# Optimization experiments

Hardware: AMD Instinct MI355X
Metric: run time of the kernel (lower is better)

## Reference

```python
import jax, jax.numpy as jnp
import numpy as np

N, E, CIN, H = 100000, 1600000, 128, 128


def setup_inputs() -> dict:
    key = jax.random.key(0)
    ks = jax.random.split(key, 10)
    return {
        "x": jax.random.normal(ks[0], (N, CIN), dtype=jnp.float32),
        "edge_index": jax.random.randint(ks[1], (2, E), 0, N, dtype=jnp.int64),
        "edge_weight": jax.random.uniform(ks[2], (E,), dtype=jnp.float32),
        "h_prev": jax.random.normal(ks[3], (N, H), dtype=jnp.float32),
        "c_prev": jax.random.normal(ks[4], (N, H), dtype=jnp.float32),
        "Wx0": jax.random.normal(ks[5], (4, CIN, H), dtype=jnp.float32) * 0.05,
        "Wx1": jax.random.normal(ks[6], (4, CIN, H), dtype=jnp.float32) * 0.05,
        "Wh0": jax.random.normal(ks[7], (4, H, H), dtype=jnp.float32) * 0.05,
        "Wh1": jax.random.normal(ks[8], (4, H, H), dtype=jnp.float32) * 0.05,
        "bx": jnp.zeros((4, H), dtype=jnp.float32),
        "bh": jnp.zeros((4, H), dtype=jnp.float32),
    }


def _scaled_laplacian_norm(edge_index, edge_weight, n):
    # PyG ChebConv norm with lambda_max=2.0, sym normalization:
    # L_hat = 2L/lambda_max - I = -D^{-1/2} A D^{-1/2} (zero diagonal).
    src, dst = edge_index[0], edge_index[1]
    deg = jax.ops.segment_sum(edge_weight, src, num_segments=n)
    safe = jnp.where(deg > 0, deg, 1.0)
    dis = jnp.where(deg > 0, 1.0 / jnp.sqrt(safe), 0.0)  # deg_inv_sqrt, inf->0
    norm = -(dis[src] * edge_weight * dis[dst])
    return src, dst, norm


def _propagate(feat, src, dst, norm, n):
    # (L_hat @ feat)[i] = sum_{e: dst_e=i} norm_e * feat[src_e]
    return jax.ops.segment_sum(feat[src] * norm[:, None], dst, num_segments=n)


def reference(x, edge_index, edge_weight, h_prev, c_prev, Wx0, Wx1, Wh0, Wh1, bx, bh):
    n = x.shape[0]
    src, dst, norm = _scaled_laplacian_norm(edge_index, edge_weight, n)
    # Shared Chebyshev propagation across all 4 gates (K=2: T0=I, T1=L_hat)
    Lx = _propagate(x, src, dst, norm, n)          # [N, CIN]
    Lh = _propagate(h_prev, src, dst, norm, n)     # [N, H]
    gates = (
        jnp.einsum("nc,gch->gnh", x, Wx0)
        + jnp.einsum("nc,gch->gnh", Lx, Wx1)
        + jnp.einsum("nd,gdh->gnh", h_prev, Wh0)
        + jnp.einsum("nd,gdh->gnh", Lh, Wh1)
        + bx[:, None, :] + bh[:, None, :]
    )  # [4, N, H]
    i = jax.nn.sigmoid(gates[0])
    f = jax.nn.sigmoid(gates[1])
    g = jnp.tanh(gates[2])
    o = jax.nn.sigmoid(gates[3])
    c_t = f * c_prev + i * g
    h_t = o * jnp.tanh(c_t)
    return (h_t, c_t)
```

## Files before the change

kernel.cpp:

```cpp
#include <hip/hip_runtime.h>
#include <hip/hip_bf16.h>

#define NN   100000
#define NE   1600000
#define MPAD 100096
#define BK   64

typedef __attribute__((ext_vector_type(8))) short bf16x8;
typedef __attribute__((ext_vector_type(4))) float f32x4;
typedef __attribute__((ext_vector_type(8))) unsigned short u16x8;

#define OFF_DEG    0ull
#define OFF_CUR    400384ull
#define OFF_XH     800768ull
#define OFF_FP     52049920ull
#define OFF_WT     103299072ull
#define OFF_BIAS   103823360ull

__device__ __forceinline__ unsigned short f2bf(float f) {
    unsigned int u = __float_as_uint(f);
    u += 0x7fffu + ((u >> 16) & 1u);
    return (unsigned short)(u >> 16);
}
__device__ __forceinline__ float bf2f(unsigned short u) {
    return __uint_as_float(((unsigned int)u) << 16);
}
__device__ __forceinline__ float sigf(float x)  { return 1.f / (1.f + __expf(-x)); }
__device__ __forceinline__ float tanhf_(float x){ return 1.f - 2.f / (__expf(2.f * x) + 1.f); }

typedef __attribute__((address_space(3))) void lds_void;
typedef __attribute__((address_space(1))) void g_void;
__device__ __forceinline__ void gload16(const void* g, void* l) {
    __builtin_amdgcn_global_load_lds((const g_void*)g, (lds_void*)l, 16, 0, 0);
}

__global__ void zero_kernel(float4* __restrict__ p, int n4) {
    int t = blockIdx.x * 256 + threadIdx.x;
    if (t < n4) p[t] = make_float4(0.f, 0.f, 0.f, 0.f);
}

#define EDGE_BLOCKS 6250
#define CVT_BLOCKS  25024
__global__ void mega1_kernel(const int* __restrict__ src, const int* __restrict__ dst,
                             const float* __restrict__ ew,
                             float* __restrict__ deg, int* __restrict__ cursor,
                             uint2* __restrict__ bkt,
                             const float* __restrict__ x, const float* __restrict__ hp,
                             unsigned short* __restrict__ XH,
                             const float* __restrict__ Wx0, const float* __restrict__ Wx1,
                             const float* __restrict__ Wh0, const float* __restrict__ Wh1,
                             const float* __restrict__ bx,  const float* __restrict__ bh,
                             unsigned short* __restrict__ Wt, float* __restrict__ bias) {
    int b = blockIdx.x;
    if (b < EDGE_BLOCKS) {
        int e = b * 256 + threadIdx.x;
        int s = src[e], d = dst[e];
        float w = ew[e];
        atomicAdd(&deg[s], w);
        int pos = atomicAdd(&cursor[d], 1);
        if (pos < BK) {
            uint2 v; v.x = (unsigned)s; v.y = __float_as_uint(w);
            bkt[((size_t)d << 6) + pos] = v;
        }
    } else if (b < EDGE_BLOCKS + CVT_BLOCKS) {
        int t = (b - EDGE_BLOCKS) * 256 + threadIdx.x;
        int n = t >> 6, q = t & 63;
        ushort4 o = make_ushort4(0, 0, 0, 0);
        if (n < NN) {
            const float* s = (q < 32) ? (x + (size_t)n * 128 + (q << 2))
                                      : (hp + (size_t)n * 128 + ((q - 32) << 2));
            float4 v = *(const float4*)s;
            o = make_ushort4(f2bf(v.x), f2bf(v.y), f2bf(v.z), f2bf(v.w));
        }
        *(ushort4*)(XH + (size_t)n * 256 + (q << 2)) = o;
    } else {
        int t = (b - EDGE_BLOCKS - CVT_BLOCKS) * 256 + threadIdx.x;
        int col = t >> 9, k = t & 511;
        int h = col >> 2, g = col & 3;
        const float* W; int kk;
        if      (k < 128) { W = Wx0; kk = k; }
        else if (k < 256) { W = Wx1; kk = k - 128; }
        else if (k < 384) { W = Wh0; kk = k - 256; }
        else              { W = Wh1; kk = k - 384; }
        float v = W[((size_t)(g << 7) + kk) * 128 + h];
        Wt[(size_t)col * 512 + k] = f2bf(v);
        if (k == 0) bias[col] = bx[(g << 7) + h] + bh[(g << 7) + h];
    }
}

__launch_bounds__(256)
__global__ void gather_pack_kernel(const float* __restrict__ deg,
                                   const int* __restrict__ cursor,
                                   const uint2* __restrict__ bkt,
                                   const unsigned short* __restrict__ XH,
                                   unsigned short* __restrict__ Fp) {
    int node = (blockIdx.x * 256 + threadIdx.x) >> 6;
    int lane = threadIdx.x & 63;
    if (node >= MPAD) return;
    const int g  = lane >> 4;
    const int li = lane & 15;
    unsigned short* Frow = Fp + (size_t)node * 256;
    if (node >= NN) {
        if (g < 2) *(uint4*)(Frow + li * 16 + g * 8) = make_uint4(0, 0, 0, 0);
        return;
    }
    int cnt = cursor[node];
    cnt = cnt > BK ? BK : cnt;
    float dd = deg[node];
    float disd = dd > 0.f ? rsqrtf(dd) : 0.f;
    const uint2* row = bkt + ((size_t)node << 6);
    float acc[16];
#pragma unroll
    for (int k = 0; k < 16; ++k) acc[k] = 0.f;

    int e = g;
    uint2 ce;
    if (e < cnt) ce = row[e];
    while (e < cnt) {
        uint2 cur = ce;
        int en = e + 4;
        if (en < cnt) ce = row[en];
        float dsv = deg[cur.x];
        const unsigned short* xr = XH + (size_t)cur.x * 256 + li * 16;
        u16x8 v0 = *(const u16x8*)(xr);
        u16x8 v1 = *(const u16x8*)(xr + 8);
        float diss = dsv > 0.f ? rsqrtf(dsv) : 0.f;
        float nm = -(diss * __uint_as_float(cur.y) * disd);
#pragma unroll
        for (int k = 0; k < 8; ++k) acc[k]     += nm * bf2f((unsigned short)v0[k]);
#pragma unroll
        for (int k = 0; k < 8; ++k) acc[k + 8] += nm * bf2f((unsigned short)v1[k]);
        e = en;
    }
#pragma unroll
    for (int k = 0; k < 16; ++k) {
        acc[k] += __shfl_xor(acc[k], 16, 64);
        acc[k] += __shfl_xor(acc[k], 32, 64);
    }
    if (g < 2) {
        u16x8 o;
#pragma unroll
        for (int k = 0; k < 8; ++k)
            o[k] = f2bf((g & 1) ? acc[k + 8] : acc[k]);
        *(u16x8*)(Frow + li * 16 + g * 8) = o;
    }
}

__device__ __forceinline__ f32x4 shflx4(f32x4 v, int m) {
    f32x4 r;
    r[0] = __shfl_xor(v[0], m, 64);
    r[1] = __shfl_xor(v[1], m, 64);
    r[2] = __shfl_xor(v[2], m, 64);
    r[3] = __shfl_xor(v[3], m, 64);
    return r;
}
__device__ __forceinline__ float sel4(f32x4 v, int k) {
    float r = v[0];
    r = (k == 1) ? v[1] : r;
    r = (k == 2) ? v[2] : r;
    r = (k == 3) ? v[3] : r;
    return r;
}
__device__ __forceinline__ float pick4(float a0, float a1, float a2, float a3, int k) {
    float r = a0;
    r = (k == 1) ? a1 : r;
    r = (k == 2) ? a2 : r;
    r = (k == 3) ? a3 : r;
    return r;
}

#define WAITV(n)  asm volatile("s_waitcnt vmcnt(" #n ")" ::: "memory")
#define WAITLGKM0 asm volatile("s_waitcnt lgkmcnt(0)" ::: "memory")

__launch_bounds__(256)
__global__ void gemm_lstm_kernel(const unsigned short* __restrict__ XHu,
                                 const unsigned short* __restrict__ Fpu,
                                 const unsigned short* __restrict__ Wtu,
                                 const float* __restrict__ bias,
                                 const float* __restrict__ c_prev,
                                 float* __restrict__ out) {
    __shared__ __align__(16) short sa[4 * 4096];
    __shared__ __align__(16) short sb[4 * 4096];

    const int tid  = threadIdx.x;
    const int lane = tid & 63;
    const int wave = tid >> 6;
    const int wm = wave >> 1, wn = wave & 1;
    const int lr = lane & 15, lq = lane >> 4;

    const int b = blockIdx.x;
    const int ntile = (b >> 3) & 3;
    const int mtile = (b & 7) | ((b >> 5) << 3);
    if (mtile >= 782) return;
    const size_t m0 = (size_t)mtile * 128;
    const int n0 = ntile * 128;

    const short* XH = (const short*)XHu;
    const short* Fp = (const short*)Fpu;
    const short* Wt = (const short*)Wtu;

    const int arow = tid >> 2;
    const int sx   = (((tid & 3) ^ ((arow >> 1) & 3)) << 3);
    const size_t rowA = (m0 + arow) * 256 + sx;
    const short* gB = Wt + (size_t)(n0 + arow) * 512 + sx;

    const int rbase = wm * 64 + lq * 4 + (lr & 3);
    const int hbase = (n0 >> 2) + wn * 16 + (lr >> 2);

    const int xr = (lr >> 1) & 3;
    int offA[4], offB[4];
#pragma unroll
    for (int i = 0; i < 4; ++i) {
        offA[i] = (wm * 64 + i * 16 + lr) * 32 + ((lq ^ xr) << 3);
        offB[i] = (wn * 64 + i * 16 + lr) * 32 + ((lq ^ xr) << 3);
    }

    f32x4 acc[4][4];
#pragma unroll
    for (int i = 0; i < 4; ++i)
#pragma unroll
        for (int j = 0; j < 4; ++j) acc[i][j] = (f32x4){0.f, 0.f, 0.f, 0.f};

    auto stage = [&](int kt) {
        const int buf = (kt & 3) << 12;
        const int off = ((kt >> 3) << 7) + ((kt & 3) << 5);
        const short* Ab = ((kt >> 2) & 1) ? Fp : XH;
        gload16(Ab + rowA + off,            &sa[buf + wave * 512]);
        gload16(Ab + rowA + 64 * 256 + off, &sa[buf + 2048 + wave * 512]);
        gload16(gB + kt * 32,               &sb[buf + wave * 512]);
        gload16(gB + kt * 32 + 64 * 512,    &sb[buf + 2048 + wave * 512]);
    };

    stage(0); stage(1); stage(2);

#pragma unroll
    for (int kt = 0; kt < 16; ++kt) {
        if      (kt <= 13) WAITV(8);
        else if (kt == 14) WAITV(4);
        else               WAITV(0);
        __builtin_amdgcn_sched_barrier(0);
        __builtin_amdgcn_s_barrier();
        if (kt + 3 < 16) stage(kt + 3);
        const int buf = (kt & 3) << 12;
        bf16x8 af[4], bfr[4];
#pragma unroll
        for (int i = 0; i < 4; ++i) af[i]  = *(const bf16x8*)&sa[buf + offA[i]];
#pragma unroll
        for (int i = 0; i < 4; ++i) bfr[i] = *(const bf16x8*)&sb[buf + offB[i]];
        __builtin_amdgcn_s_setprio(1);
#pragma unroll
        for (int i = 0; i < 4; ++i)
#pragma unroll
            for (int j = 0; j < 4; ++j)
                acc[i][j] = __builtin_amdgcn_mfma_f32_16x16x32_bf16(af[i], bfr[j], acc[i][j], 0, 0, 0);
        __builtin_amdgcn_s_setprio(0);
        WAITLGKM0;
        __builtin_amdgcn_sched_barrier(0);
    }

    float bs[4];
#pragma unroll
    for (int j = 0; j < 4; ++j) bs[j] = bias[n0 + wn * 64 + j * 16 + lr];
    float cp[4][4];
#pragma unroll
    for (int i = 0; i < 4; ++i) {
        size_t grow = m0 + rbase + i * 16;
#pragma unroll
        for (int j = 0; j < 4; ++j)
            cp[i][j] = (grow < NN) ? c_prev[grow * 128 + hbase + j * 4] : 0.f;
    }

    const int k = lr & 3;
#pragma unroll
    for (int i = 0; i < 4; ++i) {
        size_t grow = m0 + rbase + i * 16;
        if (grow >= NN) continue;
#pragma unroll
        for (int j = 0; j < 4; ++j) {
            f32x4 v0 = acc[i][j];
            v0[0] += bs[j]; v0[1] += bs[j]; v0[2] += bs[j]; v0[3] += bs[j];
            f32x4 v1 = shflx4(v0, 1);
            f32x4 v2 = shflx4(v0, 2);
            f32x4 v3 = shflx4(v0, 3);
            float vv0 = sel4(v0, k), vv1 = sel4(v1, k),
                  vv2 = sel4(v2, k), vv3 = sel4(v3, k);
            float gi = pick4(vv0, vv1, vv2, vv3, k);
            float gf = pick4(vv0, vv1, vv2, vv3, k ^ 1);
            float gg = pick4(vv0, vv1, vv2, vv3, k ^ 2);
            float go = pick4(vv0, vv1, vv2, vv3, k ^ 3);
            float iv = sigf(gi), fv = sigf(gf), gv = tanhf_(gg), ov = sigf(go);
            float ct = fv * cp[i][j] + iv * gv;
            float ht = ov * tanhf_(ct);
            int h = hbase + j * 4;
            out[grow * 128 + h] = ht;
            out[(size_t)NN * 128 + grow * 128 + h] = ct;
        }
    }
}

extern "C" void kernel_launch(void* const* d_in, const int* in_sizes, int n_in,
                              void* d_out, int out_size, void* d_ws, size_t ws_size,
                              hipStream_t stream) {
    const float* x      = (const float*)d_in[0];
    const int*   ei     = (const int*)  d_in[1];
    const float* ew     = (const float*)d_in[2];
    const float* h_prev = (const float*)d_in[3];
    const float* c_prev = (const float*)d_in[4];
    const float* Wx0    = (const float*)d_in[5];
    const float* Wx1    = (const float*)d_in[6];
    const float* Wh0    = (const float*)d_in[7];
    const float* Wh1    = (const float*)d_in[8];
    const float* bx     = (const float*)d_in[9];
    const float* bh     = (const float*)d_in[10];
    float* out = (float*)d_out;

    char* ws = (char*)d_ws;
    float*          deg    = (float*)(ws + OFF_DEG);
    int*            cursor = (int*)  (ws + OFF_CUR);
    unsigned short* XH     = (unsigned short*)(ws + OFF_XH);
    unsigned short* Fp     = (unsigned short*)(ws + OFF_FP);
    unsigned short* Wt     = (unsigned short*)(ws + OFF_WT);
    float*          bias   = (float*)(ws + OFF_BIAS);
    uint2*          bkt    = (uint2*)d_out;

    const int* src = ei;
    const int* dst = ei + NE;

    zero_kernel<<<(50048 + 255) / 256, 256, 0, stream>>>((float4*)ws, 50048);

    mega1_kernel<<<EDGE_BLOCKS + CVT_BLOCKS + 1024, 256, 0, stream>>>(
        src, dst, ew, deg, cursor, bkt, x, h_prev, XH,
        Wx0, Wx1, Wh0, Wh1, bx, bh, Wt, bias);

    gather_pack_kernel<<<MPAD / 4, 256, 0, stream>>>(deg, cursor, bkt, XH, Fp);

    gemm_lstm_kernel<<<3136, 256, 0, stream>>>(XH, Fp, Wt, bias, c_prev, out);
}
```

Before: 600.9 us.

## Split GEMM: compute unpropagated half early, overlapped with edge bucketing

```diff
diff --git a/kernel.cpp b/kernel.cpp
--- a/kernel.cpp
+++ b/kernel.cpp
@@ -10,12 +10,14 @@
 typedef __attribute__((ext_vector_type(4))) float f32x4;
 typedef __attribute__((ext_vector_type(8))) unsigned short u16x8;
 
-#define OFF_DEG    0ull
-#define OFF_CUR    400384ull
-#define OFF_XH     800768ull
-#define OFF_FP     52049920ull
-#define OFF_WT     103299072ull
-#define OFF_BIAS   103823360ull
+#define OFF_DEG  0ull
+#define OFF_CUR  400384ull
+#define OFF_XH   800768ull
+#define OFF_FP   52049920ull
+#define OFF_WT   103299072ull
+#define OFF_BIAS 103823360ull
+#define OFF_GP   103825408ull
+#define WS_NEED  206323712ull
 
 __device__ __forceinline__ unsigned short f2bf(float f) {
     unsigned int u = __float_as_uint(f);
@@ -34,26 +36,60 @@
     __builtin_amdgcn_global_load_lds((const g_void*)g, (lds_void*)l, 16, 0, 0);
 }
 
-__global__ void zero_kernel(float4* __restrict__ p, int n4) {
-    int t = blockIdx.x * 256 + threadIdx.x;
-    if (t < n4) p[t] = make_float4(0.f, 0.f, 0.f, 0.f);
-}
-
-#define EDGE_BLOCKS 6250
-#define CVT_BLOCKS  25024
-__global__ void mega1_kernel(const int* __restrict__ src, const int* __restrict__ dst,
+__global__ void zero_packw_kernel(float4* __restrict__ z,
+                                  const float* __restrict__ Wx0, const float* __restrict__ Wx1,
+                                  const float* __restrict__ Wh0, const float* __restrict__ Wh1,
+                                  const float* __restrict__ bx,  const float* __restrict__ bh,
+                                  unsigned short* __restrict__ Wt, float* __restrict__ bias) {
+    int b = blockIdx.x;
+    if (b < 196) {
+        int t = b * 256 + threadIdx.x;
+        if (t < 50048) z[t] = make_float4(0.f, 0.f, 0.f, 0.f);
+        return;
+    }
+    int t = (b - 196) * 256 + threadIdx.x;
+    int col = t >> 9, k = t & 511;
+    int h = col >> 2, g = col & 3;
+    const float* W; int kk;
+    if      (k < 128) { W = Wx0; kk = k; }
+    else if (k < 256) { W = Wx1; kk = k - 128; }
+    else if (k < 384) { W = Wh0; kk = k - 256; }
+    else              { W = Wh1; kk = k - 384; }
+    float v = W[((size_t)(g << 7) + kk) * 128 + h];
+    Wt[(size_t)col * 512 + k] = f2bf(v);
+    if (k == 0) bias[col] = bx[(g << 7) + h] + bh[(g << 7) + h];
+}
+
+#define MIX_BLOCKS 9408
+#define CVT_BLOCKS 25024
+__global__ void mega2_kernel(const int* __restrict__ src, const int* __restrict__ dst,
                              const float* __restrict__ ew,
                              float* __restrict__ deg, int* __restrict__ cursor,
                              uint2* __restrict__ bkt,
                              const float* __restrict__ x, const float* __restrict__ hp,
                              unsigned short* __restrict__ XH,
-                             const float* __restrict__ Wx0, const float* __restrict__ Wx1,
-                             const float* __restrict__ Wh0, const float* __restrict__ Wh1,
-                             const float* __restrict__ bx,  const float* __restrict__ bh,
-                             unsigned short* __restrict__ Wt, float* __restrict__ bias) {
-    int b = blockIdx.x;
-    if (b < EDGE_BLOCKS) {
-        int e = b * 256 + threadIdx.x;
+                             const unsigned short* __restrict__ Wtu,
+                             unsigned short* __restrict__ Gp,
+                             int with_g1) {
+    __shared__ __align__(16) short s1a[2][4096];
+    __shared__ __align__(16) short s1b[2][4096];
+
+    const int b = blockIdx.x;
+    int eid = -1, g1 = -1, cvt = -1;
+    if (with_g1) {
+        if (b < MIX_BLOCKS) {
+            int r = b % 3, g = b / 3;
+            if (r == 0) g1 = g;
+            else if (g < 3125) eid = (r - 1) * 3125 + g;
+            else return;
+        } else cvt = b - MIX_BLOCKS;
+    } else {
+        if (b < 6250) eid = b;
+        else cvt = b - 6250;
+    }
+
+    if (eid >= 0) {
+        int e = eid * 256 + threadIdx.x;
         int s = src[e], d = dst[e];
         float w = ew[e];
         atomicAdd(&deg[s], w);
@@ -62,8 +98,10 @@
             uint2 v; v.x = (unsigned)s; v.y = __float_as_uint(w);
             bkt[((size_t)d << 6) + pos] = v;
         }
-    } else if (b < EDGE_BLOCKS + CVT_BLOCKS) {
-        int t = (b - EDGE_BLOCKS) * 256 + threadIdx.x;
+        return;
+    }
+    if (cvt >= 0) {
+        int t = cvt * 256 + threadIdx.x;
         int n = t >> 6, q = t & 63;
         ushort4 o = make_ushort4(0, 0, 0, 0);
         if (n < NN) {
@@ -73,19 +111,98 @@
             o = make_ushort4(f2bf(v.x), f2bf(v.y), f2bf(v.z), f2bf(v.w));
         }
         *(ushort4*)(XH + (size_t)n * 256 + (q << 2)) = o;
-    } else {
-        int t = (b - EDGE_BLOCKS - CVT_BLOCKS) * 256 + threadIdx.x;
-        int col = t >> 9, k = t & 511;
-        int h = col >> 2, g = col & 3;
-        const float* W; int kk;
-        if      (k < 128) { W = Wx0; kk = k; }
-        else if (k < 256) { W = Wx1; kk = k - 128; }
-        else if (k < 384) { W = Wh0; kk = k - 256; }
-        else              { W = Wh1; kk = k - 384; }
-        float v = W[((size_t)(g << 7) + kk) * 128 + h];
-        Wt[(size_t)col * 512 + k] = f2bf(v);
-        if (k == 0) bias[col] = bx[(g << 7) + h] + bh[(g << 7) + h];
-    }
+        return;
+    }
+
+    const int ntile = (g1 >> 3) & 3;
+    const int mtile = (g1 & 7) | ((g1 >> 5) << 3);
+    if (mtile >= 782) return;
+    const size_t m0 = (size_t)mtile * 128;
+    const int n0 = ntile * 128;
+
+    const int tid  = threadIdx.x;
+    const int lane = tid & 63;
+    const int wave = tid >> 6;
+    const int wm = wave >> 1, wn = wave & 1;
+    const int lr = lane & 15, lq = lane >> 4;
+
+    const short* Wt = (const short*)Wtu;
+    const int ar  = tid >> 2;
+    const int ac  = tid & 3;
+    const int sxw = ((ac ^ ((ar >> 1) & 3)) << 3);
+    const short* gB = Wt + (size_t)(n0 + ar) * 512 + sxw;
+
+    const int xr = (lr >> 1) & 3;
+    int offA[4], offB[4];
+#pragma unroll
+    for (int i = 0; i < 4; ++i) {
+        offA[i] = (wm * 64 + i * 16 + lr) * 32 + ((lq ^ xr) << 3);
+        offB[i] = (wn * 64 + i * 16 + lr) * 32 + ((lq ^ xr) << 3);
+    }
+
+    f32x4 acc[4][4];
+#pragma unroll
+    for (int i = 0; i < 4; ++i)
+#pragma unroll
+        for (int j = 0; j < 4; ++j) acc[i][j] = (f32x4){0.f, 0.f, 0.f, 0.f};
+
+    auto ldsA = [&](int s, int buf) {
+#pragma unroll
+        for (int half = 0; half < 2; ++half) {
+            int row = ar + half * 64;
+            size_t grow = m0 + row;
+            float v[8];
+            if (grow < NN) {
+                const float* p = (s < 4 ? x + grow * 128 + s * 32
+                                        : hp + grow * 128 + (s - 4) * 32) + ac * 8;
+                float4 a0 = *(const float4*)p;
+                float4 a1 = *(const float4*)(p + 4);
+                v[0] = a0.x; v[1] = a0.y; v[2] = a0.z; v[3] = a0.w;
+                v[4] = a1.x; v[5] = a1.y; v[6] = a1.z; v[7] = a1.w;
+            } else {
+#pragma unroll
+                for (int q = 0; q < 8; ++q) v[q] = 0.f;
+            }
+            u16x8 o;
+#pragma unroll
+            for (int q = 0; q < 8; ++q) o[q] = f2bf(v[q]);
+            *(u16x8*)&s1a[buf][row * 32 + sxw] = o;
+        }
+    };
+    auto stB = [&](int s, int buf) {
+        int ktw = (s < 4) ? s : s + 4;
+        gload16(gB + ktw * 32,            &s1b[buf][wave * 512]);
+        gload16(gB + ktw * 32 + 64 * 512, &s1b[buf][2048 + wave * 512]);
+    };
+
+    stB(0, 0); ldsA(0, 0);
+    __syncthreads();
+    for (int s = 0; s < 8; ++s) {
+        const int buf = s & 1;
+        if (s < 7) { stB(s + 1, buf ^ 1); ldsA(s + 1, buf ^ 1); }
+        bf16x8 af[4], bfr[4];
+#pragma unroll
+        for (int i = 0; i < 4; ++i) af[i]  = *(const bf16x8*)&s1a[buf][offA[i]];
+#pragma unroll
+        for (int i = 0; i < 4; ++i) bfr[i] = *(const bf16x8*)&s1b[buf][offB[i]];
+#pragma unroll
+        for (int i = 0; i < 4; ++i)
+#pragma unroll
+            for (int j = 0; j < 4; ++j)
+                acc[i][j] = __builtin_amdgcn_mfma_f32_16x16x32_bf16(af[i], bfr[j], acc[i][j], 0, 0, 0);
+        __syncthreads();
+    }
+
+#pragma unroll
+    for (int i = 0; i < 4; ++i)
+#pragma unroll
+        for (int j = 0; j < 4; ++j) {
+            int col = n0 + wn * 64 + j * 16 + lr;
+            size_t rowb = m0 + wm * 64 + i * 16 + lq * 4;
+            ushort4 o = make_ushort4(f2bf(acc[i][j][0]), f2bf(acc[i][j][1]),
+                                     f2bf(acc[i][j][2]), f2bf(acc[i][j][3]));
+            *(ushort4*)(Gp + (size_t)col * MPAD + rowb) = o;
+        }
 }
 
 __launch_bounds__(256)
@@ -172,12 +289,14 @@
 #define WAITV(n)  asm volatile("s_waitcnt vmcnt(" #n ")" ::: "memory")
 #define WAITLGKM0 asm volatile("s_waitcnt lgkmcnt(0)" ::: "memory")
 
+template <int SPLIT>
 __launch_bounds__(256)
 __global__ void gemm_lstm_kernel(const unsigned short* __restrict__ XHu,
                                  const unsigned short* __restrict__ Fpu,
                                  const unsigned short* __restrict__ Wtu,
                                  const float* __restrict__ bias,
                                  const float* __restrict__ c_prev,
+                                 const unsigned short* __restrict__ Gp,
                                  float* __restrict__ out) {
     __shared__ __align__(16) short sa[4 * 4096];
     __shared__ __align__(16) short sb[4 * 4096];
@@ -215,14 +334,8 @@
         offB[i] = (wn * 64 + i * 16 + lr) * 32 + ((lq ^ xr) << 3);
     }
 
-    f32x4 acc[4][4];
-#pragma unroll
-    for (int i = 0; i < 4; ++i)
-#pragma unroll
-        for (int j = 0; j < 4; ++j) acc[i][j] = (f32x4){0.f, 0.f, 0.f, 0.f};
-
-    auto stage = [&](int kt) {
-        const int buf = (kt & 3) << 12;
+    auto stage = [&](int kt, int b4) {
+        const int buf = b4 << 12;
         const int off = ((kt >> 3) << 7) + ((kt & 3) << 5);
         const short* Ab = ((kt >> 2) & 1) ? Fp : XH;
         gload16(Ab + rowA + off,            &sa[buf + wave * 512]);
@@ -230,18 +343,43 @@
         gload16(gB + kt * 32,               &sb[buf + wave * 512]);
         gload16(gB + kt * 32 + 64 * 512,    &sb[buf + 2048 + wave * 512]);
     };
-
-    stage(0); stage(1); stage(2);
-
-#pragma unroll
-    for (int kt = 0; kt < 16; ++kt) {
-        if      (kt <= 13) WAITV(8);
-        else if (kt == 14) WAITV(4);
-        else               WAITV(0);
+    auto ktOf = [&](int s) { return SPLIT ? (s < 4 ? s + 4 : s + 8) : s; };
+    const int NS = SPLIT ? 8 : 16;
+
+    f32x4 acc[4][4];
+    if (SPLIT) {
+        ushort4 gpt[4][4];
+#pragma unroll
+        for (int i = 0; i < 4; ++i)
+#pragma unroll
+            for (int j = 0; j < 4; ++j)
+                gpt[i][j] = *(const ushort4*)(Gp +
+                    (size_t)(n0 + wn * 64 + j * 16 + lr) * MPAD +
+                    (m0 + wm * 64 + i * 16 + lq * 4));
+        stage(ktOf(0), 0); stage(ktOf(1), 1); stage(ktOf(2), 2);
+#pragma unroll
+        for (int i = 0; i < 4; ++i)
+#pragma unroll
+            for (int j = 0; j < 4; ++j)
+                acc[i][j] = (f32x4){bf2f(gpt[i][j].x), bf2f(gpt[i][j].y),
+                                    bf2f(gpt[i][j].z), bf2f(gpt[i][j].w)};
+    } else {
+#pragma unroll
+        for (int i = 0; i < 4; ++i)
+#pragma unroll
+            for (int j = 0; j < 4; ++j) acc[i][j] = (f32x4){0.f, 0.f, 0.f, 0.f};
+        stage(0, 0); stage(1, 1); stage(2, 2);
+    }
+
+#pragma unroll
+    for (int s = 0; s < NS; ++s) {
+        if      (s <= NS - 3) WAITV(8);
+        else if (s == NS - 2) WAITV(4);
+        else                  WAITV(0);
         __builtin_amdgcn_sched_barrier(0);
         __builtin_amdgcn_s_barrier();
-        if (kt + 3 < 16) stage(kt + 3);
-        const int buf = (kt & 3) << 12;
+        if (s + 3 < NS) stage(ktOf(s + 3), (s + 3) & 3);
+        const int buf = (s & 3) << 12;
         bf16x8 af[4], bfr[4];
 #pragma unroll
         for (int i = 0; i < 4; ++i) af[i]  = *(const bf16x8*)&sa[buf + offA[i]];
@@ -321,18 +459,26 @@
     unsigned short* Fp     = (unsigned short*)(ws + OFF_FP);
     unsigned short* Wt     = (unsigned short*)(ws + OFF_WT);
     float*          bias   = (float*)(ws + OFF_BIAS);
+    unsigned short* Gp     = (unsigned short*)(ws + OFF_GP);
     uint2*          bkt    = (uint2*)d_out;
 
     const int* src = ei;
     const int* dst = ei + NE;
 
-    zero_kernel<<<(50048 + 255) / 256, 256, 0, stream>>>((float4*)ws, 50048);
-
-    mega1_kernel<<<EDGE_BLOCKS + CVT_BLOCKS + 1024, 256, 0, stream>>>(
-        src, dst, ew, deg, cursor, bkt, x, h_prev, XH,
-        Wx0, Wx1, Wh0, Wh1, bx, bh, Wt, bias);
-
-    gather_pack_kernel<<<MPAD / 4, 256, 0, stream>>>(deg, cursor, bkt, XH, Fp);
-
-    gemm_lstm_kernel<<<3136, 256, 0, stream>>>(XH, Fp, Wt, bias, c_prev, out);
-}
+    const bool big = (ws_size >= WS_NEED);
+
+    zero_packw_kernel<<<196 + 1024, 256, 0, stream>>>(
+        (float4*)ws, Wx0, Wx1, Wh0, Wh1, bx, bh, Wt, bias);
+
+    if (big) {
+        mega2_kernel<<<MIX_BLOCKS + CVT_BLOCKS, 256, 0, stream>>>(
+            src, dst, ew, deg, cursor, bkt, x, h_prev, XH, Wt, Gp, 1);
+        gather_pack_kernel<<<MPAD / 4, 256, 0, stream>>>(deg, cursor, bkt, XH, Fp);
+        gemm_lstm_kernel<1><<<3136, 256, 0, stream>>>(XH, Fp, Wt, bias, c_prev, Gp, out);
+    } else {
+        mega2_kernel<<<6250 + CVT_BLOCKS, 256, 0, stream>>>(
+            src, dst, ew, deg, cursor, bkt, x, h_prev, XH, Wt, Gp, 0);
+        gather_pack_kernel<<<MPAD / 4, 256, 0, stream>>>(deg, cursor, bkt, XH, Fp);
+        gemm_lstm_kernel<0><<<3136, 256, 0, stream>>>(XH, Fp, Wt, bias, c_prev, Gp, out);
+    }
+}
```

Result: slower. 670.4 us (+11.6%).

## Widen gather edge parallelism, batch edge atomics, and move weight packing into zero kernel

Applied to the files above, without the earlier changes.

```diff
diff --git a/kernel.cpp b/kernel.cpp
--- a/kernel.cpp
+++ b/kernel.cpp
@@ -10,12 +10,12 @@
 typedef __attribute__((ext_vector_type(4))) float f32x4;
 typedef __attribute__((ext_vector_type(8))) unsigned short u16x8;
 
-#define OFF_DEG    0ull
-#define OFF_CUR    400384ull
-#define OFF_XH     800768ull
-#define OFF_FP     52049920ull
-#define OFF_WT     103299072ull
-#define OFF_BIAS   103823360ull
+#define OFF_DEG  0ull
+#define OFF_CUR  400384ull
+#define OFF_XH   800768ull
+#define OFF_FP   52049920ull
+#define OFF_WT   103299072ull
+#define OFF_BIAS 103823360ull
 
 __device__ __forceinline__ unsigned short f2bf(float f) {
     unsigned int u = __float_as_uint(f);
@@ -34,58 +34,73 @@
     __builtin_amdgcn_global_load_lds((const g_void*)g, (lds_void*)l, 16, 0, 0);
 }
 
-__global__ void zero_kernel(float4* __restrict__ p, int n4) {
-    int t = blockIdx.x * 256 + threadIdx.x;
-    if (t < n4) p[t] = make_float4(0.f, 0.f, 0.f, 0.f);
-}
-
-#define EDGE_BLOCKS 6250
-#define CVT_BLOCKS  25024
+__global__ void zero_packw_kernel(float4* __restrict__ z,
+                                  const float* __restrict__ Wx0, const float* __restrict__ Wx1,
+                                  const float* __restrict__ Wh0, const float* __restrict__ Wh1,
+                                  const float* __restrict__ bx,  const float* __restrict__ bh,
+                                  unsigned short* __restrict__ Wt, float* __restrict__ bias) {
+    int b = blockIdx.x;
+    if (b < 196) {
+        int t = b * 256 + threadIdx.x;
+        if (t < 50048) z[t] = make_float4(0.f, 0.f, 0.f, 0.f);
+        return;
+    }
+    int t = (b - 196) * 256 + threadIdx.x;
+    int col = t >> 9, k = t & 511;
+    int h = col >> 2, g = col & 3;
+    const float* W; int kk;
+    if      (k < 128) { W = Wx0; kk = k; }
+    else if (k < 256) { W = Wx1; kk = k - 128; }
+    else if (k < 384) { W = Wh0; kk = k - 256; }
+    else              { W = Wh1; kk = k - 384; }
+    float v = W[((size_t)(g << 7) + kk) * 128 + h];
+    Wt[(size_t)col * 512 + k] = f2bf(v);
+    if (k == 0) bias[col] = bx[(g << 7) + h] + bh[(g << 7) + h];
+}
+
+#define EB 1563
+#define CVT_BLOCKS 25024
 __global__ void mega1_kernel(const int* __restrict__ src, const int* __restrict__ dst,
                              const float* __restrict__ ew,
                              float* __restrict__ deg, int* __restrict__ cursor,
                              uint2* __restrict__ bkt,
                              const float* __restrict__ x, const float* __restrict__ hp,
-                             unsigned short* __restrict__ XH,
-                             const float* __restrict__ Wx0, const float* __restrict__ Wx1,
-                             const float* __restrict__ Wh0, const float* __restrict__ Wh1,
-                             const float* __restrict__ bx,  const float* __restrict__ bh,
-                             unsigned short* __restrict__ Wt, float* __restrict__ bias) {
+                             unsigned short* __restrict__ XH) {
     int b = blockIdx.x;
-    if (b < EDGE_BLOCKS) {
-        int e = b * 256 + threadIdx.x;
-        int s = src[e], d = dst[e];
-        float w = ew[e];
-        atomicAdd(&deg[s], w);
-        int pos = atomicAdd(&cursor[d], 1);
-        if (pos < BK) {
-            uint2 v; v.x = (unsigned)s; v.y = __float_as_uint(w);
-            bkt[((size_t)d << 6) + pos] = v;
+    if (b < EB) {
+        int e0 = b * 1024 + threadIdx.x;
+        int sarr[4], darr[4]; float warr[4]; bool ok[4];
+#pragma unroll
+        for (int k = 0; k < 4; ++k) {
+            int e = e0 + k * 256;
+            ok[k] = (e < NE);
+            if (ok[k]) { sarr[k] = src[e]; darr[k] = dst[e]; warr[k] = ew[e]; }
         }
-    } else if (b < EDGE_BLOCKS + CVT_BLOCKS) {
-        int t = (b - EDGE_BLOCKS) * 256 + threadIdx.x;
-        int n = t >> 6, q = t & 63;
-        ushort4 o = make_ushort4(0, 0, 0, 0);
-        if (n < NN) {
-            const float* s = (q < 32) ? (x + (size_t)n * 128 + (q << 2))
-                                      : (hp + (size_t)n * 128 + ((q - 32) << 2));
-            float4 v = *(const float4*)s;
-            o = make_ushort4(f2bf(v.x), f2bf(v.y), f2bf(v.z), f2bf(v.w));
-        }
-        *(ushort4*)(XH + (size_t)n * 256 + (q << 2)) = o;
-    } else {
-        int t = (b - EDGE_BLOCKS - CVT_BLOCKS) * 256 + threadIdx.x;
-        int col = t >> 9, k = t & 511;
-        int h = col >> 2, g = col & 3;
-        const float* W; int kk;
-        if      (k < 128) { W = Wx0; kk = k; }
-        else if (k < 256) { W = Wx1; kk = k - 128; }
-        else if (k < 384) { W = Wh0; kk = k - 256; }
-        else              { W = Wh1; kk = k - 384; }
-        float v = W[((size_t)(g << 7) + kk) * 128 + h];
-        Wt[(size_t)col * 512 + k] = f2bf(v);
-        if (k == 0) bias[col] = bx[(g << 7) + h] + bh[(g << 7) + h];
-    }
+#pragma unroll
+        for (int k = 0; k < 4; ++k)
+            if (ok[k]) atomicAdd(&deg[sarr[k]], warr[k]);
+        int pos[4];
+#pragma unroll
+        for (int k = 0; k < 4; ++k)
+            if (ok[k]) pos[k] = atomicAdd(&cursor[darr[k]], 1);
+#pragma unroll
+        for (int k = 0; k < 4; ++k)
+            if (ok[k] && pos[k] < BK) {
+                uint2 v; v.x = (unsigned)sarr[k]; v.y = __float_as_uint(warr[k]);
+                bkt[((size_t)darr[k] << 6) + pos[k]] = v;
+            }
+        return;
+    }
+    int t = (b - EB) * 256 + threadIdx.x;
+    int n = t >> 6, q = t & 63;
+    ushort4 o = make_ushort4(0, 0, 0, 0);
+    if (n < NN) {
+        const float* s = (q < 32) ? (x + (size_t)n * 128 + (q << 2))
+                                  : (hp + (size_t)n * 128 + ((q - 32) << 2));
+        float4 v = *(const float4*)s;
+        o = make_ushort4(f2bf(v.x), f2bf(v.y), f2bf(v.z), f2bf(v.w));
+    }
+    *(ushort4*)(XH + (size_t)n * 256 + (q << 2)) = o;
 }
 
 __launch_bounds__(256)
@@ -97,11 +112,11 @@
     int node = (blockIdx.x * 256 + threadIdx.x) >> 6;
     int lane = threadIdx.x & 63;
     if (node >= MPAD) return;
-    const int g  = lane >> 4;
-    const int li = lane & 15;
+    const int g  = lane >> 3;
+    const int li = lane & 7;
     unsigned short* Frow = Fp + (size_t)node * 256;
     if (node >= NN) {
-        if (g < 2) *(uint4*)(Frow + li * 16 + g * 8) = make_uint4(0, 0, 0, 0);
+        if (g < 4) *(uint4*)(Frow + li * 32 + g * 8) = make_uint4(0, 0, 0, 0);
         return;
     }
     int cnt = cursor[node];
@@ -109,40 +124,47 @@
     float dd = deg[node];
     float disd = dd > 0.f ? rsqrtf(dd) : 0.f;
     const uint2* row = bkt + ((size_t)node << 6);
-    float acc[16];
-#pragma unroll
-    for (int k = 0; k < 16; ++k) acc[k] = 0.f;
+    float acc[32];
+#pragma unroll
+    for (int k = 0; k < 32; ++k) acc[k] = 0.f;
 
     int e = g;
     uint2 ce;
     if (e < cnt) ce = row[e];
     while (e < cnt) {
         uint2 cur = ce;
-        int en = e + 4;
+        int en = e + 8;
         if (en < cnt) ce = row[en];
         float dsv = deg[cur.x];
-        const unsigned short* xr = XH + (size_t)cur.x * 256 + li * 16;
+        const unsigned short* xr = XH + (size_t)cur.x * 256 + li * 32;
         u16x8 v0 = *(const u16x8*)(xr);
         u16x8 v1 = *(const u16x8*)(xr + 8);
+        u16x8 v2 = *(const u16x8*)(xr + 16);
+        u16x8 v3 = *(const u16x8*)(xr + 24);
         float diss = dsv > 0.f ? rsqrtf(dsv) : 0.f;
         float nm = -(diss * __uint_as_float(cur.y) * disd);
 #pragma unroll
-        for (int k = 0; k < 8; ++k) acc[k]     += nm * bf2f((unsigned short)v0[k]);
-#pragma unroll
-        for (int k = 0; k < 8; ++k) acc[k + 8] += nm * bf2f((unsigned short)v1[k]);
+        for (int k = 0; k < 8; ++k) acc[k]      += nm * bf2f((unsigned short)v0[k]);
+#pragma unroll
+        for (int k = 0; k < 8; ++k) acc[k + 8]  += nm * bf2f((unsigned short)v1[k]);
+#pragma unroll
+        for (int k = 0; k < 8; ++k) acc[k + 16] += nm * bf2f((unsigned short)v2[k]);
+#pragma unroll
+        for (int k = 0; k < 8; ++k) acc[k + 24] += nm * bf2f((unsigned short)v3[k]);
         e = en;
     }
 #pragma unroll
-    for (int k = 0; k < 16; ++k) {
+    for (int k = 0; k < 32; ++k) {
+        acc[k] += __shfl_xor(acc[k], 8, 64);
         acc[k] += __shfl_xor(acc[k], 16, 64);
         acc[k] += __shfl_xor(acc[k], 32, 64);
     }
-    if (g < 2) {
+    if (g < 4) {
         u16x8 o;
 #pragma unroll
         for (int k = 0; k < 8; ++k)
-            o[k] = f2bf((g & 1) ? acc[k + 8] : acc[k]);
-        *(u16x8*)(Frow + li * 16 + g * 8) = o;
+            o[k] = f2bf(acc[g * 8 + k]);
+        *(u16x8*)(Frow + li * 32 + g * 8) = o;
     }
 }
 
@@ -326,11 +348,11 @@
     const int* src = ei;
     const int* dst = ei + NE;
 
-    zero_kernel<<<(50048 + 255) / 256, 256, 0, stream>>>((float4*)ws, 50048);
-
-    mega1_kernel<<<EDGE_BLOCKS + CVT_BLOCKS + 1024, 256, 0, stream>>>(
-        src, dst, ew, deg, cursor, bkt, x, h_prev, XH,
-        Wx0, Wx1, Wh0, Wh1, bx, bh, Wt, bias);
+    zero_packw_kernel<<<196 + 1024, 256, 0, stream>>>(
+        (float4*)ws, Wx0, Wx1, Wh0, Wh1, bx, bh, Wt, bias);
+
+    mega1_kernel<<<EB + CVT_BLOCKS, 256, 0, stream>>>(
+        src, dst, ew, deg, cursor, bkt, x, h_prev, XH);
 
     gather_pack_kernel<<<MPAD / 4, 256, 0, stream>>>(deg, cursor, bkt, XH, Fp);
 
```

Result: slower. 628.0 us (+4.5%).
